# Kernel optimization log

Hardware: AMD Instinct MI355X
Metric: run time of the kernel (lower is better)

Reference implementation:

```python
import jax, jax.numpy as jnp
import numpy as np

H, N, CH, RANK = 512, 64, 1, 1
SEQ_L = 4096


def setup_inputs() -> dict:
    key = jax.random.key(0)
    k0, k1, k2, k3, k4 = jax.random.split(key, 5)
    # A = -exp(A_real) + i*A_imag  (real_transform='exp'); HiPPO-style imag init
    A_real = jnp.log(0.5 + jax.random.uniform(k0, (H, N), dtype=jnp.float32))
    A_imag = jnp.broadcast_to(np.pi * jnp.arange(N, dtype=jnp.float32), (H, N)).copy()
    # complex params stored as (..., 2) real/imag pairs (torch.view_as_real layout)
    B = (0.5 ** 0.5) * jax.random.normal(k1, (1, H, N, 2), dtype=jnp.float32)
    C = jax.random.normal(k2, (CH, H, N, 2), dtype=jnp.float32)
    P = (0.5 ** 0.5) * jax.random.normal(k3, (RANK, H, N, 2), dtype=jnp.float32)
    # dt = exp(inv_dt) log-uniform in [1e-3, 1e-1]  (dt_transform='exp')
    lo, hi = np.log(1e-3), np.log(1e-1)
    inv_dt = (lo + (hi - lo) * jax.random.uniform(k4, (H,), dtype=jnp.float32)).astype(jnp.float32)
    return {"A_real": A_real, "A_imag": A_imag, "B": B, "C": C, "P": P,
            "inv_dt": inv_dt, "L": SEQ_L}


def _c(x):
    # view_as_complex
    return x[..., 0] + 1j * x[..., 1]


def _s4_kernel(A_real, A_imag, B, C, P, inv_dt, L):
    dt = jnp.exp(inv_dt)                       # (H,)
    A = -jnp.exp(A_real) + 1j * A_imag          # (H, N) complex64
    Bc, Cc, Pc = _c(B), _c(C), _c(P)            # (1,H,N), (CH,H,N), (R,H,N)
    Q = jnp.conj(Pc)

    Lf = L // 2 + 1
    omega = jnp.exp(-2j * jnp.pi / L) ** jnp.arange(Lf)   # FFT nodes, (Lf,)
    z = 2 * (1 - omega) / (1 + omega)                      # bilinear-transform freqs

    A_dt = A * dt[:, None]                     # (H, N)
    Bcat = jnp.concatenate([Bc, Pc], axis=0)   # (1+R, H, N)
    Ccat = jnp.concatenate([Cc, Q], axis=0)    # (CH+R, H, N)
    v = Bcat[:, None] * Ccat[None]             # (1+R, CH+R, H, N)
    v = v * dt[:, None]

    # Cauchy kernel with implicit conjugate-pair symmetry:
    #   r[a,b,h,l] = sum_n v/(z - A_dt) + conj(v)/(z - conj(A_dt))
    denom = 1.0 / (z - A_dt[..., None])                    # (H, N, Lf)
    r = jnp.einsum('abhn,hnl->abhl', v, denom)
    denom_c = 1.0 / (z - jnp.conj(A_dt)[..., None])
    r = r + jnp.einsum('abhn,hnl->abhl', jnp.conj(v), denom_c)

    # rank-1 Woodbury correction
    k_f = r[:-1, :-1] - r[:-1, -1:] * r[-1:, :-1] / (1 + r[-1:, -1:])
    k_f = k_f * 2 / (1 + omega)

    k = jnp.fft.irfft(k_f, n=L)                # (1, CH, H, L) real
    k = k[..., :L]
    return k[-1]                               # k_B: (CH, H, L)


def reference(A_real, A_imag, B, C, P, inv_dt, L):
    return _s4_kernel(A_real, A_imag, B, C, P, inv_dt, L)
```

## Files before the change

### kernel.cpp

```cpp
#include <hip/hip_runtime.h>
#include <math.h>

namespace {
constexpr int kH = 512;
constexpr int kN = 64;
constexpr int kL = 4096;
constexpr int kM = 2048;
constexpr int kPairRec = 40;
constexpr int kFusedThreads = 512;
constexpr float kPi = 3.14159265358979323846f;
}

typedef float v2f __attribute__((ext_vector_type(2)));

__device__ __forceinline__ int lpad(int i) { return i + (i >> 4); }
__device__ __forceinline__ v2f fma2(v2f a, v2f b, v2f c) {
    return __builtin_elementwise_fma(a, b, c);
}
__device__ __forceinline__ float2 cmul(float2 a, float2 b) {
    return make_float2(a.x*b.x - a.y*b.y, a.x*b.y + a.y*b.x);
}

__global__ __launch_bounds__(64)
void s4_prep(const float* __restrict__ A_real, const float* __restrict__ A_imag,
             const float* __restrict__ Bv, const float* __restrict__ Cv,
             const float* __restrict__ Pv, const float* __restrict__ inv_dt,
             float* __restrict__ cst, float* __restrict__ xnyq)
{
    const int h = blockIdx.x;
    const int n = threadIdx.x;
    const int idx = h * kN + n;
    const float dt = expf(inv_dt[h]);
    const float ar = -expf(A_real[idx]) * dt;
    const float ai =  A_imag[idx] * dt;
    const float br = Bv[idx*2+0], bi = Bv[idx*2+1];
    const float cr = Cv[idx*2+0], ci = Cv[idx*2+1];
    const float pr = Pv[idx*2+0], pi = Pv[idx*2+1];
    const float v00r = (br*cr - bi*ci)*dt, v00i = (br*ci + bi*cr)*dt;
    const float v01r = (br*pr + bi*pi)*dt, v01i = (bi*pr - br*pi)*dt;
    const float v10r = (pr*cr - pi*ci)*dt, v10i = (pr*ci + pi*cr)*dt;
    const float v11r = (pr*pr + pi*pi)*dt;
    const float ar2 = ar*ar;
    const float C1  = ar2 + ai*ai;
    const float dd  = ar2 - ai*ai;

    float co[16];
    co[0]  = -2.f*C1*(v00r*ar + v00i*ai);   co[1]  = 2.f*(v00i*ai - v00r*ar);
    co[2]  = -4.f*v00r*dd - 8.f*v00i*ar*ai; co[3]  = -4.f*v00r;
    co[4]  = -2.f*C1*(v01r*ar + v01i*ai);   co[5]  = 2.f*(v01i*ai - v01r*ar);
    co[6]  = -4.f*v01r*dd - 8.f*v01i*ar*ai; co[7]  = -4.f*v01r;
    co[8]  = -2.f*C1*(v10r*ar + v10i*ai);   co[9]  = 2.f*(v10i*ai - v10r*ar);
    co[10] = -4.f*v10r*dd - 8.f*v10i*ar*ai; co[11] = -4.f*v10r;
    co[12] = -2.f*C1*(v11r*ar);             co[13] = -2.f*v11r*ar;
    co[14] = -4.f*v11r*dd;                  co[15] = -4.f*v11r;

    float* base = cst + ((size_t)h * (kN/2) + (n >> 1)) * kPairRec + (n & 1);
    base[0] = ai;
    base[2] = ar2;
    #pragma unroll
    for (int k = 0; k < 16; ++k) base[4 + 2*k] = co[k];

    float s = v00r;
    #pragma unroll
    for (int off = 32; off > 0; off >>= 1) s += __shfl_down(s, off, 64);
    if (n == 0) xnyq[h] = s;
}

__global__ __launch_bounds__(kFusedThreads)
void s4_spec_ifft(const float* __restrict__ cst, const float* __restrict__ xnyq,
                  float* __restrict__ out)
{
    __shared__ float2 XS[kM];
    __shared__ float2 W2[kM + kM / 16];
    __shared__ float2 TW[kM / 2 + kM / 32];

    const int h   = blockIdx.x;
    const int tid = threadIdx.x;

    for (int j = tid; j < kM / 2; j += kFusedThreads) {
        float s, c;
        sincosf((2.0f * kPi / (float)kM) * (float)j, &s, &c);
        TW[lpad(j)] = make_float2(c, s);
    }

    const v2f* rec = (const v2f*)(cst + (size_t)h * (kN/2) * kPairRec);
    #pragma unroll 1
    for (int pass = 0; pass < 2; ++pass) {
        const int la = pass * 1024 + tid;

        float tvb[2], svb[2];
        v2f t2p[2];
        #pragma unroll
        for (int bb = 0; bb < 2; ++bb) {
            const int l = la + 512 * bb;
            float sn, cn;
            sincosf((float)l * (kPi / (float)kL), &sn, &cn);
            tvb[bb] = sn / cn;
            const float t2 = 2.f * tvb[bb];
            svb[bb] = t2 * t2;
            t2p[bb] = (v2f){t2, t2};
        }

        v2f A0[2][4], A1[2][4], B0[2][4], B1[2][4];
        #pragma unroll
        for (int bb = 0; bb < 2; ++bb)
            #pragma unroll
            for (int p = 0; p < 4; ++p) {
                A0[bb][p] = (v2f){0.f, 0.f}; A1[bb][p] = (v2f){0.f, 0.f};
                B0[bb][p] = (v2f){0.f, 0.f}; B1[bb][p] = (v2f){0.f, 0.f};
            }

        #pragma unroll 2
        for (int j = 0; j < kN/2; ++j) {
            const v2f* r = rec + j * (kPairRec/2);
            const v2f aip  = r[0];
            const v2f ar2p = r[1];
            #pragma unroll
            for (int bb = 0; bb < 2; ++bb) {
                const v2f w1 = t2p[bb] - aip;
                const v2f w2 = t2p[bb] + aip;
                const v2f m1 = fma2(w1, w1, ar2p);
                const v2f m2 = fma2(w2, w2, ar2p);
                const v2f D  = m1 * m2;
                const float qq = __builtin_amdgcn_rcpf(D.x * D.y);
                v2f qv;
                qv.x = D.y * qq;
                qv.y = D.x * qq;
                #pragma unroll
                for (int p = 0; p < 4; ++p) {
                    A0[bb][p] = fma2(r[2 + 4*p + 0], qv, A0[bb][p]);
                    A1[bb][p] = fma2(r[2 + 4*p + 1], qv, A1[bb][p]);
                    B0[bb][p] = fma2(r[2 + 4*p + 2], qv, B0[bb][p]);
                    B1[bb][p] = fma2(r[2 + 4*p + 3], qv, B1[bb][p]);
                }
            }
        }

        #pragma unroll
        for (int bb = 0; bb < 2; ++bb) {
            const int l = la + 512 * bb;
            const float t = tvb[bb];
            const v2f sp = (v2f){svb[bb], svb[bb]};
            const v2f r00 = fma2(sp, A1[bb][0], A0[bb][0]);
            const v2f i00 = fma2(sp, B1[bb][0], B0[bb][0]);
            const v2f r01 = fma2(sp, A1[bb][1], A0[bb][1]);
            const v2f i01 = fma2(sp, B1[bb][1], B0[bb][1]);
            const v2f r10 = fma2(sp, A1[bb][2], A0[bb][2]);
            const v2f i10 = fma2(sp, B1[bb][2], B0[bb][2]);
            const v2f r11 = fma2(sp, A1[bb][3], A0[bb][3]);
            const v2f i11 = fma2(sp, B1[bb][3], B0[bb][3]);
            const float s00r = r00.x + r00.y, s00i = t * (i00.x + i00.y);
            const float s01r = r01.x + r01.y, s01i = t * (i01.x + i01.y);
            const float s10r = r10.x + r10.y, s10i = t * (i10.x + i10.y);
            const float s11r = r11.x + r11.y, s11i = t * (i11.x + i11.y);
            const float nr = s01r*s10r - s01i*s10i;
            const float ni = s01r*s10i + s01i*s10r;
            const float dr = 1.f + s11r, di = s11i;
            const float qd = __builtin_amdgcn_rcpf(fmaf(dr, dr, di*di));
            const float wr = (nr*dr + ni*di) * qd;
            const float wi = (ni*dr - nr*di) * qd;
            const float gr = s00r - wr, gi = s00i - wi;
            XS[l] = make_float2(fmaf(-gi, t, gr), fmaf(gr, t, gi));
        }
    }
    __syncthreads();

    const float nyqR = xnyq[h];
    for (int k = tid; k <= kM / 2; k += kFusedThreads) {
        const float2 Xa = XS[k];
        const float2 Xb = (k == 0) ? make_float2(nyqR, 0.0f) : XS[kM - k];
        const float Er = 0.5f * (Xa.x + Xb.x);
        const float Ei = 0.5f * (Xa.y - Xb.y);
        const float Dr = 0.5f * (Xa.x - Xb.x);
        const float Di = 0.5f * (Xa.y + Xb.y);
        float s, c;
        sincosf((2.0f * kPi / (float)kL) * (float)k, &s, &c);
        const float Or = c * Dr - s * Di;
        const float Oi = c * Di + s * Dr;
        const int rk = (int)(__brev((unsigned)k) >> 21);
        W2[lpad(rk)] = make_float2(Er - Oi, Ei + Or);
        if (k != 0 && k != kM / 2) {
            const int rmk = (int)(__brev((unsigned)(kM - k)) >> 21);
            W2[lpad(rmk)] = make_float2(Er + Oi, Or - Ei);
        }
    }
    __syncthreads();

    for (int j = tid; j < kM / 4; j += kFusedThreads) {
        const int i0 = j * 4;
        const float2 e0 = W2[lpad(i0)];
        const float2 e1 = W2[lpad(i0 + 1)];
        const float2 e2 = W2[lpad(i0 + 2)];
        const float2 e3 = W2[lpad(i0 + 3)];
        const float2 a0 = make_float2(e0.x + e1.x, e0.y + e1.y);
        const float2 a1 = make_float2(e0.x - e1.x, e0.y - e1.y);
        const float2 a2 = make_float2(e2.x + e3.x, e2.y + e3.y);
        const float2 a3 = make_float2(e2.x - e3.x, e2.y - e3.y);
        W2[lpad(i0)]     = make_float2(a0.x + a2.x, a0.y + a2.y);
        W2[lpad(i0 + 2)] = make_float2(a0.x - a2.x, a0.y - a2.y);
        W2[lpad(i0 + 1)] = make_float2(a1.x - a3.y, a1.y + a3.x);
        W2[lpad(i0 + 3)] = make_float2(a1.x + a3.y, a1.y - a3.x);
    }
    __syncthreads();

    #pragma unroll
    for (int lg = 2; lg <= 8; lg += 2) {
        const int hs = 1 << lg;
        const int twstride = 512 >> lg;
        for (int j = tid; j < kM / 4; j += kFusedThreads) {
            const int pos = j & (hs - 1);
            const int grp = j >> lg;
            const int i0  = grp * 4 * hs + pos;
            const float2 e0 = W2[lpad(i0)];
            const float2 e1 = W2[lpad(i0 + hs)];
            const float2 e2 = W2[lpad(i0 + 2*hs)];
            const float2 e3 = W2[lpad(i0 + 3*hs)];
            const float2 wB = TW[lpad(pos * twstride)];
            const float2 wA = cmul(wB, wB);
            const float2 t1 = cmul(wA, e1);
            const float2 t3 = cmul(wA, e3);
            const float2 a0 = make_float2(e0.x + t1.x, e0.y + t1.y);
            const float2 a1 = make_float2(e0.x - t1.x, e0.y - t1.y);
            const float2 a2 = make_float2(e2.x + t3.x, e2.y + t3.y);
            const float2 a3 = make_float2(e2.x - t3.x, e2.y - t3.y);
            const float2 u2 = cmul(wB, a2);
            const float2 u3 = cmul(wB, a3);
            W2[lpad(i0)]        = make_float2(a0.x + u2.x, a0.y + u2.y);
            W2[lpad(i0 + 2*hs)] = make_float2(a0.x - u2.x, a0.y - u2.y);
            W2[lpad(i0 + hs)]   = make_float2(a1.x - u3.y, a1.y + u3.x);
            W2[lpad(i0 + 3*hs)] = make_float2(a1.x + u3.y, a1.y - u3.x);
        }
        __syncthreads();
    }
    for (int j = tid; j < kM / 2; j += kFusedThreads) {
        const float2 tw = TW[lpad(j)];
        const float2 a  = W2[lpad(j)];
        const float2 b  = W2[lpad(j + 1024)];
        const float2 tb = cmul(tw, b);
        W2[lpad(j)]        = make_float2(a.x + tb.x, a.y + tb.y);
        W2[lpad(j + 1024)] = make_float2(a.x - tb.x, a.y - tb.y);
    }
    __syncthreads();

    const float invM = 1.0f / (float)kM;
    float2* out2 = (float2*)(out + (size_t)h * kL);
    for (int n = tid; n < kM; n += kFusedThreads) {
        const float2 zn = W2[lpad(n)];
        out2[n] = make_float2(zn.x * invM, zn.y * invM);
    }
}

extern "C" void kernel_launch(void* const* d_in, const int* in_sizes, int n_in,
                              void* d_out, int out_size, void* d_ws, size_t ws_size,
                              hipStream_t stream) {
    const float* A_real = (const float*)d_in[0];
    const float* A_imag = (const float*)d_in[1];
    const float* B      = (const float*)d_in[2];
    const float* C      = (const float*)d_in[3];
    const float* P      = (const float*)d_in[4];
    const float* inv_dt = (const float*)d_in[5];
    float* out = (float*)d_out;

    float* cst  = (float*)d_ws;
    float* xnyq = cst + (size_t)kH * (kN/2) * kPairRec;

    s4_prep<<<dim3(kH), dim3(64), 0, stream>>>(A_real, A_imag, B, C, P, inv_dt,
                                               cst, xnyq);
    s4_spec_ifft<<<dim3(kH), dim3(kFusedThreads), 0, stream>>>(cst, xnyq, out);
}
```

Measured before the change: 106.2 us.

## Fuse prep into spectral kernel with LDS coefficients and 1024-thread blocks

Folds the per-head coefficient preparation into the main kernel. The first 64 threads compute the Cauchy coefficients straight into shared memory, so there is no global workspace round trip and no second launch. The block also grows from 512 to 1024 threads, each handling one pass of two frequencies instead of two passes. This removes a launch and the global reads of the coefficients, but the larger block with many accumulators may hit register limits and lower occupancy. Coefficient reads in the inner loop are now LDS broadcasts instead of cached global loads.

```diff
diff --git a/kernel.cpp b/kernel.cpp
--- a/kernel.cpp
+++ b/kernel.cpp
@@ -7,7 +7,7 @@
 constexpr int kL = 4096;
 constexpr int kM = 2048;
 constexpr int kPairRec = 40;
-constexpr int kFusedThreads = 512;
+constexpr int kThreads = 1024;
 constexpr float kPi = 3.14159265358979323846f;
 }
 
@@ -21,55 +21,14 @@
     return make_float2(a.x*b.x - a.y*b.y, a.x*b.y + a.y*b.x);
 }
 
-__global__ __launch_bounds__(64)
-void s4_prep(const float* __restrict__ A_real, const float* __restrict__ A_imag,
-             const float* __restrict__ Bv, const float* __restrict__ Cv,
-             const float* __restrict__ Pv, const float* __restrict__ inv_dt,
-             float* __restrict__ cst, float* __restrict__ xnyq)
+__global__ __launch_bounds__(kThreads)
+void s4_all(const float* __restrict__ A_real, const float* __restrict__ A_imag,
+            const float* __restrict__ Bv, const float* __restrict__ Cv,
+            const float* __restrict__ Pv, const float* __restrict__ inv_dt,
+            float* __restrict__ out)
 {
-    const int h = blockIdx.x;
-    const int n = threadIdx.x;
-    const int idx = h * kN + n;
-    const float dt = expf(inv_dt[h]);
-    const float ar = -expf(A_real[idx]) * dt;
-    const float ai =  A_imag[idx] * dt;
-    const float br = Bv[idx*2+0], bi = Bv[idx*2+1];
-    const float cr = Cv[idx*2+0], ci = Cv[idx*2+1];
-    const float pr = Pv[idx*2+0], pi = Pv[idx*2+1];
-    const float v00r = (br*cr - bi*ci)*dt, v00i = (br*ci + bi*cr)*dt;
-    const float v01r = (br*pr + bi*pi)*dt, v01i = (bi*pr - br*pi)*dt;
-    const float v10r = (pr*cr - pi*ci)*dt, v10i = (pr*ci + pi*cr)*dt;
-    const float v11r = (pr*pr + pi*pi)*dt;
-    const float ar2 = ar*ar;
-    const float C1  = ar2 + ai*ai;
-    const float dd  = ar2 - ai*ai;
-
-    float co[16];
-    co[0]  = -2.f*C1*(v00r*ar + v00i*ai);   co[1]  = 2.f*(v00i*ai - v00r*ar);
-    co[2]  = -4.f*v00r*dd - 8.f*v00i*ar*ai; co[3]  = -4.f*v00r;
-    co[4]  = -2.f*C1*(v01r*ar + v01i*ai);   co[5]  = 2.f*(v01i*ai - v01r*ar);
-    co[6]  = -4.f*v01r*dd - 8.f*v01i*ar*ai; co[7]  = -4.f*v01r;
-    co[8]  = -2.f*C1*(v10r*ar + v10i*ai);   co[9]  = 2.f*(v10i*ai - v10r*ar);
-    co[10] = -4.f*v10r*dd - 8.f*v10i*ar*ai; co[11] = -4.f*v10r;
-    co[12] = -2.f*C1*(v11r*ar);             co[13] = -2.f*v11r*ar;
-    co[14] = -4.f*v11r*dd;                  co[15] = -4.f*v11r;
-
-    float* base = cst + ((size_t)h * (kN/2) + (n >> 1)) * kPairRec + (n & 1);
-    base[0] = ai;
-    base[2] = ar2;
-    #pragma unroll
-    for (int k = 0; k < 16; ++k) base[4 + 2*k] = co[k];
-
-    float s = v00r;
-    #pragma unroll
-    for (int off = 32; off > 0; off >>= 1) s += __shfl_down(s, off, 64);
-    if (n == 0) xnyq[h] = s;
-}
-
-__global__ __launch_bounds__(kFusedThreads)
-void s4_spec_ifft(const float* __restrict__ cst, const float* __restrict__ xnyq,
-                  float* __restrict__ out)
-{
+    __shared__ v2f    CREC[(kN/2) * kPairRec / 2];
+    __shared__ float  sNyq;
     __shared__ float2 XS[kM];
     __shared__ float2 W2[kM + kM / 16];
     __shared__ float2 TW[kM / 2 + kM / 32];
@@ -77,22 +36,60 @@
     const int h   = blockIdx.x;
     const int tid = threadIdx.x;
 
-    for (int j = tid; j < kM / 2; j += kFusedThreads) {
+    for (int j = tid; j < kM / 2; j += kThreads) {
         float s, c;
         sincosf((2.0f * kPi / (float)kM) * (float)j, &s, &c);
         TW[lpad(j)] = make_float2(c, s);
     }
 
-    const v2f* rec = (const v2f*)(cst + (size_t)h * (kN/2) * kPairRec);
-    #pragma unroll 1
-    for (int pass = 0; pass < 2; ++pass) {
-        const int la = pass * 1024 + tid;
+    if (tid < kN) {
+        const int n = tid;
+        const int idx = h * kN + n;
+        const float dt = expf(inv_dt[h]);
+        const float ar = -expf(A_real[idx]) * dt;
+        const float ai =  A_imag[idx] * dt;
+        const float br = Bv[idx*2+0], bi = Bv[idx*2+1];
+        const float cr = Cv[idx*2+0], ci = Cv[idx*2+1];
+        const float pr = Pv[idx*2+0], pi = Pv[idx*2+1];
+        const float v00r = (br*cr - bi*ci)*dt, v00i = (br*ci + bi*cr)*dt;
+        const float v01r = (br*pr + bi*pi)*dt, v01i = (bi*pr - br*pi)*dt;
+        const float v10r = (pr*cr - pi*ci)*dt, v10i = (pr*ci + pi*cr)*dt;
+        const float v11r = (pr*pr + pi*pi)*dt;
+        const float ar2 = ar*ar;
+        const float C1  = ar2 + ai*ai;
+        const float dd  = ar2 - ai*ai;
+
+        float co[16];
+        co[0]  = -2.f*C1*(v00r*ar + v00i*ai);   co[1]  = 2.f*(v00i*ai - v00r*ar);
+        co[2]  = -4.f*v00r*dd - 8.f*v00i*ar*ai; co[3]  = -4.f*v00r;
+        co[4]  = -2.f*C1*(v01r*ar + v01i*ai);   co[5]  = 2.f*(v01i*ai - v01r*ar);
+        co[6]  = -4.f*v01r*dd - 8.f*v01i*ar*ai; co[7]  = -4.f*v01r;
+        co[8]  = -2.f*C1*(v10r*ar + v10i*ai);   co[9]  = 2.f*(v10i*ai - v10r*ar);
+        co[10] = -4.f*v10r*dd - 8.f*v10i*ar*ai; co[11] = -4.f*v10r;
+        co[12] = -2.f*C1*(v11r*ar);             co[13] = -2.f*v11r*ar;
+        co[14] = -4.f*v11r*dd;                  co[15] = -4.f*v11r;
+
+        float* base = (float*)CREC + (size_t)(n >> 1) * kPairRec + (n & 1);
+        base[0] = ai;
+        base[2] = ar2;
+        #pragma unroll
+        for (int k = 0; k < 16; ++k) base[4 + 2*k] = co[k];
+
+        float s = v00r;
+        #pragma unroll
+        for (int off = 32; off > 0; off >>= 1) s += __shfl_down(s, off, 64);
+        if (n == 0) sNyq = s;
+    }
+    __syncthreads();
+
+    {
+        const int la = tid;
 
         float tvb[2], svb[2];
         v2f t2p[2];
         #pragma unroll
         for (int bb = 0; bb < 2; ++bb) {
-            const int l = la + 512 * bb;
+            const int l = la + 1024 * bb;
             float sn, cn;
             sincosf((float)l * (kPi / (float)kL), &sn, &cn);
             tvb[bb] = sn / cn;
@@ -112,7 +109,7 @@
 
         #pragma unroll 2
         for (int j = 0; j < kN/2; ++j) {
-            const v2f* r = rec + j * (kPairRec/2);
+            const v2f* r = CREC + j * (kPairRec/2);
             const v2f aip  = r[0];
             const v2f ar2p = r[1];
             #pragma unroll
@@ -138,7 +135,7 @@
 
         #pragma unroll
         for (int bb = 0; bb < 2; ++bb) {
-            const int l = la + 512 * bb;
+            const int l = la + 1024 * bb;
             const float t = tvb[bb];
             const v2f sp = (v2f){svb[bb], svb[bb]};
             const v2f r00 = fma2(sp, A1[bb][0], A0[bb][0]);
@@ -165,8 +162,8 @@
     }
     __syncthreads();
 
-    const float nyqR = xnyq[h];
-    for (int k = tid; k <= kM / 2; k += kFusedThreads) {
+    const float nyqR = sNyq;
+    for (int k = tid; k <= kM / 2; k += kThreads) {
         const float2 Xa = XS[k];
         const float2 Xb = (k == 0) ? make_float2(nyqR, 0.0f) : XS[kM - k];
         const float Er = 0.5f * (Xa.x + Xb.x);
@@ -186,7 +183,7 @@
     }
     __syncthreads();
 
-    for (int j = tid; j < kM / 4; j += kFusedThreads) {
+    for (int j = tid; j < kM / 4; j += kThreads) {
         const int i0 = j * 4;
         const float2 e0 = W2[lpad(i0)];
         const float2 e1 = W2[lpad(i0 + 1)];
@@ -207,7 +204,7 @@
     for (int lg = 2; lg <= 8; lg += 2) {
         const int hs = 1 << lg;
         const int twstride = 512 >> lg;
-        for (int j = tid; j < kM / 4; j += kFusedThreads) {
+        for (int j = tid; j < kM / 4; j += kThreads) {
             const int pos = j & (hs - 1);
             const int grp = j >> lg;
             const int i0  = grp * 4 * hs + pos;
@@ -232,7 +229,7 @@
         }
         __syncthreads();
     }
-    for (int j = tid; j < kM / 2; j += kFusedThreads) {
+    for (int j = tid; j < kM / 2; j += kThreads) {
         const float2 tw = TW[lpad(j)];
         const float2 a  = W2[lpad(j)];
         const float2 b  = W2[lpad(j + 1024)];
@@ -244,7 +241,7 @@
 
     const float invM = 1.0f / (float)kM;
     float2* out2 = (float2*)(out + (size_t)h * kL);
-    for (int n = tid; n < kM; n += kFusedThreads) {
+    for (int n = tid; n < kM; n += kThreads) {
         const float2 zn = W2[lpad(n)];
         out2[n] = make_float2(zn.x * invM, zn.y * invM);
     }
@@ -261,10 +258,6 @@
     const float* inv_dt = (const float*)d_in[5];
     float* out = (float*)d_out;
 
-    float* cst  = (float*)d_ws;
-    float* xnyq = cst + (size_t)kH * (kN/2) * kPairRec;
-
-    s4_prep<<<dim3(kH), dim3(64), 0, stream>>>(A_real, A_imag, B, C, P, inv_dt,
-                                               cst, xnyq);
-    s4_spec_ifft<<<dim3(kH), dim3(kFusedThreads), 0, stream>>>(cst, xnyq, out);
-}
+    s4_all<<<dim3(kH), dim3(kThreads), 0, stream>>>(A_real, A_imag, B, C, P,
+                                                    inv_dt, out);
+}
```

New measurement: 106.1 us. About the same (-0.1%).
